# Performance work log

Measured on AMD Instinct MI355X. Metric: run time of the kernel, lower is better.

The kernel has to match this reference:

```python
import jax, jax.numpy as jnp
import numpy as np

B = 65536
D_EMB = 512      # embedding_dim
D_SPD = 1        # speed_dim
D_LAT = 128      # speed_latent_dim
H = 256          # hidden_size
K = 6            # num_branch
D_IN = D_EMB + D_LAT  # 640, branch/speed-head input dim


def _lin(key, din, dout):
    kw, kb = jax.random.split(key)
    W = jax.random.normal(kw, (din, dout), dtype=jnp.float32) * 0.02
    b = jax.random.normal(kb, (dout,), dtype=jnp.float32) * 0.02
    return W, b


def setup_inputs() -> dict:
    key = jax.random.key(0)
    ks = jax.random.split(key, 16)
    embedding = jax.random.normal(ks[0], (B, D_EMB), dtype=jnp.float32)
    speed = jax.random.uniform(ks[1], (B, D_SPD), dtype=jnp.float32)
    command = jax.random.randint(ks[2], (B,), 1, K + 1, dtype=jnp.int32)  # values 1..6
    # speed input MLP: speed_dim -> H -> D_LAT
    Wsi1, bsi1 = _lin(ks[3], D_SPD, H)
    Wsi2, bsi2 = _lin(ks[4], H, D_LAT)
    # speed prediction head: D_IN -> H -> H -> speed_dim
    Wso1, bso1 = _lin(ks[5], D_IN, H)
    Wso2, bso2 = _lin(ks[6], H, H)
    Wso3, bso3 = _lin(ks[7], H, D_SPD)
    # K branch heads, stacked on leading axis: D_IN -> H -> H -> 3, sigmoid
    def _stack(key, din, dout):
        kw, kb = jax.random.split(key)
        W = jax.random.normal(kw, (K, din, dout), dtype=jnp.float32) * 0.02
        b = jax.random.normal(kb, (K, dout), dtype=jnp.float32) * 0.02
        return W, b
    Wb1, bb1 = _stack(ks[8], D_IN, H)
    Wb2, bb2 = _stack(ks[9], H, H)
    Wb3, bb3 = _stack(ks[10], H, 3)
    return dict(embedding=embedding, speed=speed, command=command,
                Wsi1=Wsi1, bsi1=bsi1, Wsi2=Wsi2, bsi2=bsi2,
                Wso1=Wso1, bso1=bso1, Wso2=Wso2, bso2=bso2, Wso3=Wso3, bso3=bso3,
                Wb1=Wb1, bb1=bb1, Wb2=Wb2, bb2=bb2, Wb3=Wb3, bb3=bb3)


def reference(embedding, speed, command,
              Wsi1, bsi1, Wsi2, bsi2,
              Wso1, bso1, Wso2, bso2, Wso3, bso3,
              Wb1, bb1, Wb2, bb2, Wb3, bb3):
    # speed -> latent
    sp = jax.nn.relu(speed @ Wsi1 + bsi1) @ Wsi2 + bsi2          # [B, D_LAT]
    emb = jnp.concatenate([embedding, sp], axis=1)               # [B, D_IN]
    # compute ALL K branch heads (as the original does), then mask by command
    h = jax.nn.relu(jnp.einsum('bd,kdh->bkh', emb, Wb1) + bb1)   # [B, K, H]
    h = jax.nn.relu(jnp.einsum('bkh,khj->bkj', h, Wb2) + bb2)    # [B, K, H]
    ctrl_all = jax.nn.sigmoid(jnp.einsum('bkh,kho->bko', h, Wb3) + bb3)  # [B, K, 3]
    mask = (command[:, None] - 1 == jnp.arange(K)[None, :]).astype(ctrl_all.dtype)  # [B, K]
    control_pred = jnp.sum(ctrl_all * mask[:, :, None], axis=1)  # [B, 3]
    # speed prediction head
    hs = jax.nn.relu(emb @ Wso1 + bso1)
    hs = jax.nn.relu(hs @ Wso2 + bso2)
    speed_pred = hs @ Wso3 + bso3                                # [B, 1]
    return control_pred, speed_pred
```

## Files before the change

kernel.cpp:

```cpp
#include <hip/hip_runtime.h>
#include <hip/hip_bf16.h>


#define NB 65536
#define NBRB 1030

typedef __attribute__((ext_vector_type(8))) short short8;
typedef __attribute__((ext_vector_type(4))) float f32x4;
typedef unsigned short bhalf;
typedef unsigned int u32;

__device__ __forceinline__ bhalf f2b(float x) {
    __hip_bfloat16 h = __float2bfloat16(x);
    return *reinterpret_cast<bhalf*>(&h);
}
__device__ __forceinline__ void gll16(const void* g, void* l) {
    __builtin_amdgcn_global_load_lds(
        (const __attribute__((address_space(1))) u32*)g,
        (__attribute__((address_space(3))) u32*)l, 16, 0, 0);
}
__device__ __forceinline__ int sadr(int row, int cb) {
    return row * 64 + (cb ^ (((row >> 1) & 3) << 4));
}
__device__ __forceinline__ int yadr(int row, int cb) {
    return row * 512 + (cb ^ ((row & 7) << 4));
}
__device__ __forceinline__ void wvm6() { asm volatile("s_waitcnt vmcnt(6)" ::: "memory"); }
__device__ __forceinline__ void wvm0() { asm volatile("s_waitcnt vmcnt(0)" ::: "memory"); }
__device__ __forceinline__ void wlgkm0() { asm volatile("s_waitcnt lgkmcnt(0)" ::: "memory"); }

__global__ __launch_bounds__(256) void k_wprep(
    const float* __restrict__ Wsi2, const float* __restrict__ Wso1,
    const float* __restrict__ Wso2, const float* __restrict__ Wb1,
    const float* __restrict__ Wb2,
    bhalf* __restrict__ Wsi2T, bhalf* __restrict__ Wso1T,
    bhalf* __restrict__ Wso2T, bhalf* __restrict__ Wb1T,
    bhalf* __restrict__ Wb2T) {
    __shared__ float T[64][65];
    const int id = blockIdx.x, t = threadIdx.x;
    const float* src; bhalf* dst; int K, N, tk, tn, b;
    if (id < 8)        { src = Wsi2; dst = Wsi2T; K = 256; N = 128; b = 0; int tl = id;      tk = tl / 2; tn = tl % 2; }
    else if (id < 48)  { src = Wso1; dst = Wso1T; K = 640; N = 256; b = 0; int tl = id - 8;  tk = tl / 4; tn = tl % 4; }
    else if (id < 64)  { src = Wso2; dst = Wso2T; K = 256; N = 256; b = 0; int tl = id - 48; tk = tl / 4; tn = tl % 4; }
    else if (id < 304) { src = Wb1;  dst = Wb1T;  K = 640; N = 256; int li = id - 64;  b = li / 40; int tl = li % 40; tk = tl / 4; tn = tl % 4; }
    else               { src = Wb2;  dst = Wb2T;  K = 256; N = 256; int li = id - 304; b = li / 16; int tl = li % 16; tk = tl / 4; tn = tl % 4; }
    const int k0 = tk * 64, n0 = tn * 64;
    src += (size_t)b * K * N; dst += (size_t)b * N * K;
    const int c = t & 63, r0 = t >> 6;
#pragma unroll
    for (int j = 0; j < 16; ++j) {
        int r = r0 + j * 4;
        T[r][c] = src[(size_t)(k0 + r) * N + n0 + c];
    }
    __syncthreads();
#pragma unroll
    for (int j = 0; j < 16; ++j) {
        int r = r0 + j * 4;
        dst[(size_t)(n0 + r) * K + k0 + c] = f2b(T[c][r]);
    }
}

__global__ __launch_bounds__(256) void k_prep(
    const float* __restrict__ speed, const float* __restrict__ Wsi1,
    const float* __restrict__ bsi1, const bhalf* __restrict__ Wsi2T,
    const float* __restrict__ bsi2, const int* __restrict__ cmd,
    bhalf* __restrict__ spb, int* __restrict__ bcnt) {
    __shared__ bhalf A[64 * 72];
    __shared__ bhalf BT[128 * 72];
    const int t = threadIdx.x, lane = t & 63, wid = t >> 6;
    const int rbase = blockIdx.x * 64;
    if (wid == 0) {
        int c = cmd[rbase + lane] - 1;
        int v = 0;
#pragma unroll
        for (int g = 0; g < 6; ++g) {
            unsigned long long m = __ballot(c == g);
            if (lane == g) v = (int)__popcll(m);
        }
        if (lane < 6) bcnt[blockIdx.x * 6 + lane] = v;
    }
    const int wm = wid >> 1, wn = wid & 1;
    f32x4 acc[2][4];
    for (int m = 0; m < 2; ++m) for (int n = 0; n < 4; ++n)
        for (int r = 0; r < 4; ++r) acc[m][n][r] = 0.f;
    const int ar = t >> 2, kp = (t & 3) * 16;
    const float s = speed[rbase + ar];
    for (int kc = 0; kc < 4; ++kc) {
        short8 w0, w1;
#pragma unroll
        for (int j = 0; j < 8; ++j) {
            int k = kc * 64 + kp + j;
            w0[j] = (short)f2b(fmaxf(fmaf(s, Wsi1[k], bsi1[k]), 0.f));
            w1[j] = (short)f2b(fmaxf(fmaf(s, Wsi1[k + 8], bsi1[k + 8]), 0.f));
        }
        *(short8*)&A[ar * 72 + kp] = w0;
        *(short8*)&A[ar * 72 + kp + 8] = w1;
#pragma unroll
        for (int j = 0; j < 4; ++j) {
            int ch = t + j * 256;
            int n2 = ch >> 3, ko = (ch & 7) * 8;
            *(short8*)&BT[n2 * 72 + ko] =
                *(const short8*)(Wsi2T + n2 * 256 + kc * 64 + ko);
        }
        __syncthreads();
#pragma unroll
        for (int ks = 0; ks < 2; ++ks) {
            short8 a[2], b[4];
#pragma unroll
            for (int m = 0; m < 2; ++m)
                a[m] = *(const short8*)&A[(wm * 32 + m * 16 + (lane & 15)) * 72 + ks * 32 + (lane >> 4) * 8];
#pragma unroll
            for (int n = 0; n < 4; ++n)
                b[n] = *(const short8*)&BT[(wn * 64 + n * 16 + (lane & 15)) * 72 + ks * 32 + (lane >> 4) * 8];
#pragma unroll
            for (int m = 0; m < 2; ++m)
#pragma unroll
                for (int n = 0; n < 4; ++n)
                    acc[m][n] = __builtin_amdgcn_mfma_f32_16x16x32_bf16(a[m], b[n], acc[m][n], 0, 0, 0);
        }
        __syncthreads();
    }
#pragma unroll
    for (int m = 0; m < 2; ++m)
#pragma unroll
    for (int n = 0; n < 4; ++n) {
        int col = wn * 64 + n * 16 + (lane & 15);
        float bias = bsi2[col];
#pragma unroll
        for (int r = 0; r < 4; ++r) {
            int row = rbase + wm * 32 + m * 16 + (lane >> 4) * 4 + r;
            spb[row * 128 + col] = f2b(acc[m][n][r] + bias);
        }
    }
}

__global__ __launch_bounds__(1024) void k_scan(
    const int* __restrict__ bcnt, int* __restrict__ chunkoff,
    int* __restrict__ pad) {
    __shared__ int sc[1024];
    __shared__ int tot[8];
    __shared__ int spo[8];
    const int t = threadIdx.x;
    for (int g = 0; g < 6; ++g) {
        int v = bcnt[t * 6 + g];
        sc[t] = v;
        __syncthreads();
        for (int s = 1; s < 1024; s <<= 1) {
            int u = (t >= s) ? sc[t - s] : 0;
            __syncthreads();
            sc[t] += u;
            __syncthreads();
        }
        if (t == 1023) tot[g] = sc[t];
        chunkoff[t * 6 + g] = sc[t] - v;
        __syncthreads();
    }
    if (t == 0) {
        int off = 0;
        for (int g = 0; g < 6; ++g) {
            spo[g] = off; pad[g] = off; pad[8 + g] = tot[g];
            off += ((tot[g] + 63) >> 6) << 6;
        }
        spo[6] = off; pad[6] = off;
    }
    __syncthreads();
    for (int g = 0; g < 6; ++g) chunkoff[t * 6 + g] += spo[g];
}

__global__ __launch_bounds__(256) void k_scatter(
    const int* __restrict__ cmd, const int* __restrict__ chunkoff,
    int* __restrict__ perm) {
    const int lane = threadIdx.x & 63, w = threadIdx.x >> 6;
    const int chunk = blockIdx.x * 4 + w;
    const int idx = chunk * 64 + lane;
    const int c = cmd[idx] - 1;
#pragma unroll
    for (int g = 0; g < 6; ++g) {
        unsigned long long m = __ballot(c == g);
        if (c == g) {
            int pos = chunkoff[chunk * 6 + g] + (int)__popcll(m & ((1ull << lane) - 1ull));
            perm[pos] = idx;
        }
    }
}

__global__ __launch_bounds__(256, 3) void k_head(
    const float* __restrict__ emb, const bhalf* __restrict__ spb,
    const bhalf* __restrict__ Wso1T, const float* __restrict__ bso1,
    const bhalf* __restrict__ Wso2T, const float* __restrict__ bso2,
    const float* __restrict__ Wso3, const float* __restrict__ bso3,
    const bhalf* __restrict__ Wb1T, const float* __restrict__ bb1,
    const bhalf* __restrict__ Wb2T, const float* __restrict__ bb2,
    const float* __restrict__ Wb3, const float* __restrict__ bb3,
    const int* __restrict__ pad, const int* __restrict__ perm,
    float* __restrict__ out) {
    __shared__ __align__(16) char L[49152];
    char* const SB0 = L;
    char* const SAr = L + 32768;
    char* const Yb  = L;
    const int t = threadIdx.x, lane = t & 63, wid = t >> 6;
    const bool isB = blockIdx.x < NBRB;
    int tstart, DOUT, gcnt, gbase;
    const bhalf *W1T, *W2T; const float *b1, *b2, *W3, *b3;
    if (isB) {
        tstart = blockIdx.x * 64;
        if (tstart >= pad[6]) return;
        int g = 0;
        while (pad[g + 1] <= tstart) ++g;
        gbase = pad[g]; gcnt = pad[8 + g];
        W1T = Wb1T + (size_t)g * (256 * 640); b1 = bb1 + g * 256;
        W2T = Wb2T + (size_t)g * (256 * 256); b2 = bb2 + g * 256;
        W3  = Wb3  + (size_t)g * (256 * 3);   b3 = bb3 + g * 3;
        DOUT = 3;
    } else {
        tstart = (blockIdx.x - NBRB) * 64;
        gbase = 0; gcnt = NB;
        W1T = Wso1T; b1 = bso1; W2T = Wso2T; b2 = bso2; W3 = Wso3; b3 = bso3;
        DOUT = 1;
    }

    const int rowA0 = t >> 3, rowA1 = rowA0 + 32, rowS = t >> 2;
    int ra0, ra1, raS;
    if (isB) {
        int p0 = tstart + rowA0, p1 = tstart + rowA1, pS = tstart + rowS;
        ra0 = ((p0 - gbase) < gcnt) ? perm[p0] : 0;
        ra1 = ((p1 - gbase) < gcnt) ? perm[p1] : 0;
        raS = ((pS - gbase) < gcnt) ? perm[pS] : 0;
    } else {
        ra0 = tstart + rowA0; ra1 = tstart + rowA1; raS = tstart + rowS;
    }
    const int lcA0 = ((t & 7) * 16) ^ ((rowA0 & 7) << 4);
    const int lcA1 = ((t & 7) * 16) ^ ((rowA1 & 7) << 4);
    const int lcS  = ((t & 3) * 16) ^ (((rowS >> 1) & 3) << 4);
    const char* embp0 = (const char*)(emb + (size_t)ra0 * 512);
    const char* embp1 = (const char*)(emb + (size_t)ra1 * 512);
    const char* spbp  = (const char*)(spb + (size_t)raS * 128);
    const int dstA = t * 16;
    const int rB = t >> 2, cB = (t & 3) * 16;

#define ST_A(KN, BUF) do { int kn_ = (KN); char* d_ = SAr + (BUF) * 8192 + dstA; \
        if (kn_ < 16) {                                                           \
            gll16(embp0 + kn_ * 128 + lcA0, d_);                                  \
            gll16(embp1 + kn_ * 128 + lcA1, d_ + 4096);                           \
        } else {                                                                  \
            gll16(spbp + (kn_ - 16) * 64 + lcS, d_);                              \
            gll16(spbp + (kn_ - 16) * 64 + lcS, d_ + 4096);                       \
        } } while (0)
#define ST_B1(KN, BUF) do {                                                       \
        _Pragma("unroll")                                                         \
        for (int j_ = 0; j_ < 4; ++j_) {                                          \
            int row_ = rB + j_ * 64;                                              \
            int p_ = row_ * 64 + cB;                                              \
            int lc_ = cB ^ (((row_ >> 1) & 3) << 4);                              \
            gll16((const char*)W1T + (size_t)row_ * 1280 + (KN) * 64 + lc_,       \
                  SB0 + (BUF) * 16384 + p_);                                      \
        } } while (0)
#define ST_B2(KB) do {                                                            \
        _Pragma("unroll")                                                         \
        for (int j_ = 0; j_ < 4; ++j_) {                                          \
            int row_ = rB + j_ * 64;                                              \
            int p_ = row_ * 64 + cB;                                              \
            int lc_ = cB ^ (((row_ >> 1) & 3) << 4);                              \
            gll16((const char*)W2T + (size_t)row_ * 512 + (KB) + lc_,             \
                  SAr + p_);                                                      \
        } } while (0)

    const int arow = lane & 15, koff = (lane >> 4) * 16;
    float bi1[4], bi2[4];
#pragma unroll
    for (int n = 0; n < 4; ++n) {
        bi1[n] = b1[wid * 64 + n * 16 + arow];
        bi2[n] = b2[wid * 64 + n * 16 + arow];
    }

    f32x4 acc[4][4];
#pragma unroll
    for (int m = 0; m < 4; ++m)
#pragma unroll
        for (int n = 0; n < 4; ++n)
#pragma unroll
            for (int r = 0; r < 4; ++r) acc[m][n][r] = 0.f;

    ST_A(0, 0); ST_B1(0, 0);
    for (int kc = 0; kc < 20; ++kc) {
        const int buf = kc & 1;
        if (kc < 19) { ST_A(kc + 1, buf ^ 1); ST_B1(kc + 1, buf ^ 1); wvm6(); }
        else         { wvm0(); }
        __builtin_amdgcn_s_barrier();
        const char* SAc = SAr + buf * 8192;
        const char* SBc = SB0 + buf * 16384;
        short8 a[4], b[4];
#pragma unroll
        for (int n = 0; n < 4; ++n)
            b[n] = *(const short8*)(SBc + sadr(wid * 64 + n * 16 + arow, koff));
        if (kc < 16) {
#pragma unroll
            for (int m = 0; m < 4; ++m) {
                int row = m * 16 + arow;
                int sw = (row & 7) << 4;
                int c0 = (lane >> 4) * 32;
                float4 f0 = *(const float4*)(SAc + row * 128 + (c0 ^ sw));
                float4 f1 = *(const float4*)(SAc + row * 128 + ((c0 + 16) ^ sw));
                a[m][0] = (short)f2b(f0.x); a[m][1] = (short)f2b(f0.y);
                a[m][2] = (short)f2b(f0.z); a[m][3] = (short)f2b(f0.w);
                a[m][4] = (short)f2b(f1.x); a[m][5] = (short)f2b(f1.y);
                a[m][6] = (short)f2b(f1.z); a[m][7] = (short)f2b(f1.w);
            }
        } else {
#pragma unroll
            for (int m = 0; m < 4; ++m)
                a[m] = *(const short8*)(SAc + sadr(m * 16 + arow, koff));
        }
#pragma unroll
        for (int m = 0; m < 4; ++m)
#pragma unroll
            for (int n = 0; n < 4; ++n)
                acc[m][n] = __builtin_amdgcn_mfma_f32_16x16x32_bf16(a[m], b[n], acc[m][n], 0, 0, 0);
        __builtin_amdgcn_s_barrier();
    }
#pragma unroll
    for (int m = 0; m < 4; ++m)
#pragma unroll
    for (int n = 0; n < 4; ++n) {
        int col = wid * 64 + n * 16 + arow;
#pragma unroll
        for (int r = 0; r < 4; ++r) {
            int row = m * 16 + (lane >> 4) * 4 + r;
            *(bhalf*)(Yb + yadr(row, 2 * col)) = f2b(fmaxf(acc[m][n][r] + bi1[n], 0.f));
            acc[m][n][r] = 0.f;
        }
    }
    ST_B2(0);
    wlgkm0();
    wvm0();
    __builtin_amdgcn_s_barrier();
    for (int kc = 0; kc < 8; ++kc) {
        short8 a[4], b[4];
#pragma unroll
        for (int m = 0; m < 4; ++m)
            a[m] = *(const short8*)(Yb + yadr(m * 16 + arow, kc * 64 + koff));
#pragma unroll
        for (int n = 0; n < 4; ++n)
            b[n] = *(const short8*)(SAr + sadr(wid * 64 + n * 16 + arow, koff));
#pragma unroll
        for (int m = 0; m < 4; ++m)
#pragma unroll
            for (int n = 0; n < 4; ++n)
                acc[m][n] = __builtin_amdgcn_mfma_f32_16x16x32_bf16(a[m], b[n], acc[m][n], 0, 0, 0);
        __builtin_amdgcn_s_barrier();
        if (kc < 7) { ST_B2((kc + 1) * 64); wvm0(); }
        __builtin_amdgcn_s_barrier();
    }
#pragma unroll
    for (int m = 0; m < 4; ++m)
#pragma unroll
    for (int n = 0; n < 4; ++n) {
        int col = wid * 64 + n * 16 + arow;
#pragma unroll
        for (int r = 0; r < 4; ++r) {
            int row = m * 16 + (lane >> 4) * 4 + r;
            *(bhalf*)(Yb + yadr(row, 2 * col)) = f2b(fmaxf(acc[m][n][r] + bi2[n], 0.f));
        }
    }
    wlgkm0();
    __builtin_amdgcn_s_barrier();
    f32x4 z;
#pragma unroll
    for (int r = 0; r < 4; ++r) z[r] = 0.f;
    const int col3 = arow;
    for (int kc = 0; kc < 8; ++kc) {
        short8 a3 = *(const short8*)(Yb + yadr(wid * 16 + arow, kc * 64 + koff));
        short8 bw;
#pragma unroll
        for (int j = 0; j < 8; ++j) bw[j] = 0;
        if (col3 < DOUT) {
            int kb = kc * 32 + (lane >> 4) * 8;
#pragma unroll
            for (int j = 0; j < 8; ++j)
                bw[j] = (short)f2b(W3[(kb + j) * DOUT + col3]);
        }
        z = __builtin_amdgcn_mfma_f32_16x16x32_bf16(a3, bw, z, 0, 0, 0);
    }
    if (col3 < DOUT) {
        float bias = b3[col3];
#pragma unroll
        for (int rr = 0; rr < 4; ++rr) {
            int r = wid * 16 + (lane >> 4) * 4 + rr;
            int p2 = tstart + r;
            if ((p2 - gbase) < gcnt) {
                float v = z[rr] + bias;
                if (isB) {
                    int ro = perm[p2];
                    out[(size_t)ro * 3 + col3] = 1.f / (1.f + __expf(-v));
                } else {
                    out[(size_t)NB * 3 + p2] = v;
                }
            }
        }
    }
#undef ST_A
#undef ST_B1
#undef ST_B2
}

extern "C" void kernel_launch(void* const* d_in, const int* in_sizes, int n_in,
                              void* d_out, int out_size, void* d_ws, size_t ws_size,
                              hipStream_t stream) {
    (void)in_sizes; (void)n_in; (void)out_size; (void)ws_size;
    const float* emb   = (const float*)d_in[0];
    const float* speed = (const float*)d_in[1];
    const int*   cmd   = (const int*)d_in[2];
    const float* Wsi1  = (const float*)d_in[3];
    const float* bsi1  = (const float*)d_in[4];
    const float* Wsi2  = (const float*)d_in[5];
    const float* bsi2  = (const float*)d_in[6];
    const float* Wso1  = (const float*)d_in[7];
    const float* bso1  = (const float*)d_in[8];
    const float* Wso2  = (const float*)d_in[9];
    const float* bso2  = (const float*)d_in[10];
    const float* Wso3  = (const float*)d_in[11];
    const float* bso3  = (const float*)d_in[12];
    const float* Wb1   = (const float*)d_in[13];
    const float* bb1   = (const float*)d_in[14];
    const float* Wb2   = (const float*)d_in[15];
    const float* bb2   = (const float*)d_in[16];
    const float* Wb3   = (const float*)d_in[17];
    const float* bb3   = (const float*)d_in[18];
    float* out = (float*)d_out;

    char* ws = (char*)d_ws;
    bhalf* spb      = (bhalf*)(ws);
    int*   perm     = (int*)(ws + 16777216);
    int*   bcnt     = (int*)(ws + 17040896);
    int*   chunkoff = (int*)(ws + 17065472);
    int*   pad      = (int*)(ws + 17090048);
    bhalf* Wsi2T    = (bhalf*)(ws + 17090304);
    bhalf* Wso1T    = (bhalf*)(ws + 17155840);
    bhalf* Wso2T    = (bhalf*)(ws + 17483520);
    bhalf* Wb1T     = (bhalf*)(ws + 17614592);
    bhalf* Wb2T     = (bhalf*)(ws + 19580672);

    k_wprep<<<400, 256, 0, stream>>>(Wsi2, Wso1, Wso2, Wb1, Wb2,
                                     Wsi2T, Wso1T, Wso2T, Wb1T, Wb2T);
    k_prep<<<NB / 64, 256, 0, stream>>>(speed, Wsi1, bsi1, Wsi2T, bsi2, cmd,
                                        spb, bcnt);
    k_scan<<<1, 1024, 0, stream>>>(bcnt, chunkoff, pad);
    k_scatter<<<NB / 256, 256, 0, stream>>>(cmd, chunkoff, perm);
    k_head<<<NBRB + NB / 64, 256, 0, stream>>>(emb, spb,
                                               Wso1T, bso1, Wso2T, bso2, Wso3, bso3,
                                               Wb1T, bb1, Wb2T, bb2, Wb3, bb3,
                                               pad, perm, out);
}
```

Measured before the change: 155.7 us.

## Share embedding tile loads between branch and speed heads, split into two persistent kernels

The single head kernel ran separate blocks for the branch MLP and the speed MLP, so each embedding row was loaded and converted twice. Now one block computes both first-layer GEMMs (branch and speed weights side by side, N=512) over the permuted row order. It writes the bf16 hidden activations to a global scratch buffer, and a second persistent kernel runs layers 2 and 3 for both heads. This removes the duplicate reads of the fp32 embedding. The cost is a 128 MB round-trip of intermediates, more LDS, occupancy dropping from 3 to 2 blocks, and a launch split into two grid-strided persistent grids.

```diff
diff --git a/kernel.cpp b/kernel.cpp
--- a/kernel.cpp
+++ b/kernel.cpp
@@ -3,7 +3,7 @@
 
 
 #define NB 65536
-#define NBRB 1030
+#define KGRID 1024
 
 typedef __attribute__((ext_vector_type(8))) short short8;
 typedef __attribute__((ext_vector_type(4))) float f32x4;
@@ -22,12 +22,12 @@
 __device__ __forceinline__ int sadr(int row, int cb) {
     return row * 64 + (cb ^ (((row >> 1) & 3) << 4));
 }
-__device__ __forceinline__ int yadr(int row, int cb) {
-    return row * 512 + (cb ^ ((row & 7) << 4));
-}
-__device__ __forceinline__ void wvm6() { asm volatile("s_waitcnt vmcnt(6)" ::: "memory"); }
-__device__ __forceinline__ void wvm0() { asm volatile("s_waitcnt vmcnt(0)" ::: "memory"); }
-__device__ __forceinline__ void wlgkm0() { asm volatile("s_waitcnt lgkmcnt(0)" ::: "memory"); }
+__device__ __forceinline__ int yadr2(int row, int cb) {
+    return row * 1024 + (cb ^ ((row & 7) << 4));
+}
+__device__ __forceinline__ void wvm10() { asm volatile("s_waitcnt vmcnt(10)" ::: "memory"); }
+__device__ __forceinline__ void wvm0()  { asm volatile("s_waitcnt vmcnt(0)"  ::: "memory"); }
+__device__ __forceinline__ void wlgkm0(){ asm volatile("s_waitcnt lgkmcnt(0)" ::: "memory"); }
 
 __global__ __launch_bounds__(256) void k_wprep(
     const float* __restrict__ Wsi2, const float* __restrict__ Wso1,
@@ -184,61 +184,41 @@
     }
 }
 
-__global__ __launch_bounds__(256, 3) void k_head(
+__global__ __launch_bounds__(256, 2) void k1(
     const float* __restrict__ emb, const bhalf* __restrict__ spb,
     const bhalf* __restrict__ Wso1T, const float* __restrict__ bso1,
-    const bhalf* __restrict__ Wso2T, const float* __restrict__ bso2,
-    const float* __restrict__ Wso3, const float* __restrict__ bso3,
     const bhalf* __restrict__ Wb1T, const float* __restrict__ bb1,
-    const bhalf* __restrict__ Wb2T, const float* __restrict__ bb2,
-    const float* __restrict__ Wb3, const float* __restrict__ bb3,
     const int* __restrict__ pad, const int* __restrict__ perm,
-    float* __restrict__ out) {
-    __shared__ __align__(16) char L[49152];
-    char* const SB0 = L;
-    char* const SAr = L + 32768;
-    char* const Yb  = L;
+    bhalf* __restrict__ Yg) {
+    __shared__ __align__(16) char L[81920];
+    char* const SA0 = L;
+    char* const SB0 = L + 16384;
     const int t = threadIdx.x, lane = t & 63, wid = t >> 6;
-    const bool isB = blockIdx.x < NBRB;
-    int tstart, DOUT, gcnt, gbase;
-    const bhalf *W1T, *W2T; const float *b1, *b2, *W3, *b3;
-    if (isB) {
-        tstart = blockIdx.x * 64;
-        if (tstart >= pad[6]) return;
-        int g = 0;
-        while (pad[g + 1] <= tstart) ++g;
-        gbase = pad[g]; gcnt = pad[8 + g];
-        W1T = Wb1T + (size_t)g * (256 * 640); b1 = bb1 + g * 256;
-        W2T = Wb2T + (size_t)g * (256 * 256); b2 = bb2 + g * 256;
-        W3  = Wb3  + (size_t)g * (256 * 3);   b3 = bb3 + g * 3;
-        DOUT = 3;
-    } else {
-        tstart = (blockIdx.x - NBRB) * 64;
-        gbase = 0; gcnt = NB;
-        W1T = Wso1T; b1 = bso1; W2T = Wso2T; b2 = bso2; W3 = Wso3; b3 = bso3;
-        DOUT = 1;
-    }
-
+    const int pad6 = pad[6];
+    const int arow = lane & 15, koff = (lane >> 4) * 16;
     const int rowA0 = t >> 3, rowA1 = rowA0 + 32, rowS = t >> 2;
-    int ra0, ra1, raS;
-    if (isB) {
-        int p0 = tstart + rowA0, p1 = tstart + rowA1, pS = tstart + rowS;
-        ra0 = ((p0 - gbase) < gcnt) ? perm[p0] : 0;
-        ra1 = ((p1 - gbase) < gcnt) ? perm[p1] : 0;
-        raS = ((pS - gbase) < gcnt) ? perm[pS] : 0;
-    } else {
-        ra0 = tstart + rowA0; ra1 = tstart + rowA1; raS = tstart + rowS;
-    }
     const int lcA0 = ((t & 7) * 16) ^ ((rowA0 & 7) << 4);
     const int lcA1 = ((t & 7) * 16) ^ ((rowA1 & 7) << 4);
     const int lcS  = ((t & 3) * 16) ^ (((rowS >> 1) & 3) << 4);
-    const char* embp0 = (const char*)(emb + (size_t)ra0 * 512);
-    const char* embp1 = (const char*)(emb + (size_t)ra1 * 512);
-    const char* spbp  = (const char*)(spb + (size_t)raS * 128);
     const int dstA = t * 16;
     const int rB = t >> 2, cB = (t & 3) * 16;
 
-#define ST_A(KN, BUF) do { int kn_ = (KN); char* d_ = SAr + (BUF) * 8192 + dstA; \
+    for (int tile = blockIdx.x; tile * 64 < pad6; tile += KGRID) {
+        const int tstart = tile * 64;
+        int g = 0;
+        while (pad[g + 1] <= tstart) ++g;
+        const int gbase = pad[g], gcnt = pad[8 + g];
+        const bhalf* W1b = Wb1T + (size_t)g * (256 * 640);
+
+        int p0 = tstart + rowA0, p1 = tstart + rowA1, pS = tstart + rowS;
+        const int ra0 = ((p0 - gbase) < gcnt) ? perm[p0] : 0;
+        const int ra1 = ((p1 - gbase) < gcnt) ? perm[p1] : 0;
+        const int raS = ((pS - gbase) < gcnt) ? perm[pS] : 0;
+        const char* embp0 = (const char*)(emb + (size_t)ra0 * 512);
+        const char* embp1 = (const char*)(emb + (size_t)ra1 * 512);
+        const char* spbp  = (const char*)(spb + (size_t)raS * 128);
+
+#define ST_A(KN, BUF) do { int kn_ = (KN); char* d_ = SA0 + (BUF) * 8192 + dstA; \
         if (kn_ < 16) {                                                           \
             gll16(embp0 + kn_ * 128 + lcA0, d_);                                  \
             gll16(embp1 + kn_ * 128 + lcA1, d_ + 4096);                           \
@@ -246,161 +226,245 @@
             gll16(spbp + (kn_ - 16) * 64 + lcS, d_);                              \
             gll16(spbp + (kn_ - 16) * 64 + lcS, d_ + 4096);                       \
         } } while (0)
-#define ST_B1(KN, BUF) do {                                                       \
+#define ST_B(KN, BUF) do {                                                        \
         _Pragma("unroll")                                                         \
         for (int j_ = 0; j_ < 4; ++j_) {                                          \
             int row_ = rB + j_ * 64;                                              \
             int p_ = row_ * 64 + cB;                                              \
             int lc_ = cB ^ (((row_ >> 1) & 3) << 4);                              \
-            gll16((const char*)W1T + (size_t)row_ * 1280 + (KN) * 64 + lc_,       \
-                  SB0 + (BUF) * 16384 + p_);                                      \
+            gll16((const char*)W1b + (size_t)row_ * 1280 + (KN) * 64 + lc_,       \
+                  SB0 + (BUF) * 32768 + p_);                                      \
+            gll16((const char*)Wso1T + (size_t)row_ * 1280 + (KN) * 64 + lc_,     \
+                  SB0 + (BUF) * 32768 + 16384 + p_);                              \
         } } while (0)
-#define ST_B2(KB) do {                                                            \
+
+        float bi1[8];
+#pragma unroll
+        for (int n = 0; n < 4; ++n) {
+            bi1[n]     = bb1[g * 256 + wid * 64 + n * 16 + arow];
+            bi1[n + 4] = bso1[wid * 64 + n * 16 + arow];
+        }
+
+        f32x4 acc[4][8];
+#pragma unroll
+        for (int m = 0; m < 4; ++m)
+#pragma unroll
+            for (int n = 0; n < 8; ++n)
+#pragma unroll
+                for (int r = 0; r < 4; ++r) acc[m][n][r] = 0.f;
+
+        ST_A(0, 0); ST_B(0, 0);
+        for (int kc = 0; kc < 20; ++kc) {
+            const int buf = kc & 1;
+            if (kc < 19) { ST_A(kc + 1, buf ^ 1); ST_B(kc + 1, buf ^ 1); wvm10(); }
+            else         { wvm0(); }
+            __builtin_amdgcn_s_barrier();
+            const char* SAc = SA0 + buf * 8192;
+            const char* SBc = SB0 + buf * 32768;
+            short8 a[4], b[8];
+#pragma unroll
+            for (int n = 0; n < 4; ++n) {
+                b[n]     = *(const short8*)(SBc + sadr(wid * 64 + n * 16 + arow, koff));
+                b[n + 4] = *(const short8*)(SBc + 16384 + sadr(wid * 64 + n * 16 + arow, koff));
+            }
+            if (kc < 16) {
+#pragma unroll
+                for (int m = 0; m < 4; ++m) {
+                    int row = m * 16 + arow;
+                    int sw = (row & 7) << 4;
+                    int c0 = (lane >> 4) * 32;
+                    float4 f0 = *(const float4*)(SAc + row * 128 + (c0 ^ sw));
+                    float4 f1 = *(const float4*)(SAc + row * 128 + ((c0 + 16) ^ sw));
+                    a[m][0] = (short)f2b(f0.x); a[m][1] = (short)f2b(f0.y);
+                    a[m][2] = (short)f2b(f0.z); a[m][3] = (short)f2b(f0.w);
+                    a[m][4] = (short)f2b(f1.x); a[m][5] = (short)f2b(f1.y);
+                    a[m][6] = (short)f2b(f1.z); a[m][7] = (short)f2b(f1.w);
+                }
+            } else {
+#pragma unroll
+                for (int m = 0; m < 4; ++m)
+                    a[m] = *(const short8*)(SAc + sadr(m * 16 + arow, koff));
+            }
+#pragma unroll
+            for (int m = 0; m < 4; ++m)
+#pragma unroll
+                for (int n = 0; n < 8; ++n)
+                    acc[m][n] = __builtin_amdgcn_mfma_f32_16x16x32_bf16(a[m], b[n], acc[m][n], 0, 0, 0);
+            __builtin_amdgcn_s_barrier();
+        }
+#pragma unroll
+        for (int m = 0; m < 4; ++m)
+#pragma unroll
+        for (int n = 0; n < 8; ++n) {
+            int col = (n < 4) ? (wid * 64 + n * 16 + arow)
+                              : (256 + wid * 64 + (n - 4) * 16 + arow);
+#pragma unroll
+            for (int r = 0; r < 4; ++r) {
+                int row = m * 16 + (lane >> 4) * 4 + r;
+                *(bhalf*)(L + yadr2(row, 2 * col)) = f2b(fmaxf(acc[m][n][r] + bi1[n], 0.f));
+            }
+        }
+        wlgkm0();
+        __builtin_amdgcn_s_barrier();
+        char* Ygb = (char*)Yg + (size_t)tstart * 1024;
+#pragma unroll
+        for (int j = 0; j < 16; ++j) {
+            int p = t * 16 + j * 4096;
+            int row = p >> 10, cb = p & 1023;
+            uint4 v = *(const uint4*)(L + row * 1024 + (cb ^ ((row & 7) << 4)));
+            *(uint4*)(Ygb + (size_t)row * 1024 + cb) = v;
+        }
+        __syncthreads();
+#undef ST_A
+#undef ST_B
+    }
+}
+
+__global__ __launch_bounds__(256, 2) void k2(
+    const bhalf* __restrict__ Yg,
+    const bhalf* __restrict__ Wso2T, const float* __restrict__ bso2,
+    const float* __restrict__ Wso3, const float* __restrict__ bso3,
+    const bhalf* __restrict__ Wb2T, const float* __restrict__ bb2,
+    const float* __restrict__ Wb3, const float* __restrict__ bb3,
+    const int* __restrict__ pad, const int* __restrict__ perm,
+    float* __restrict__ out) {
+    __shared__ __align__(16) char L[81920];
+    char* const SA0 = L;
+    char* const SB0 = L + 16384;
+    const int t = threadIdx.x, lane = t & 63, wid = t >> 6;
+    const int pad6 = pad[6];
+    const int arow = lane & 15, koff = (lane >> 4) * 16;
+    const int rowY = t >> 2, cA = (t & 3) * 16;
+    const int lcA = cA ^ (((rowY >> 1) & 3) << 4);
+    const int dstA = t * 16;
+    const int rB = t >> 2, cB = (t & 3) * 16;
+
+    for (int tile = blockIdx.x; tile * 64 < pad6; tile += KGRID) {
+        const int tstart = tile * 64;
+        int g = 0;
+        while (pad[g + 1] <= tstart) ++g;
+        const int gbase = pad[g], gcnt = pad[8 + g];
+        const bhalf* W2b = Wb2T + (size_t)g * (256 * 256);
+        const float* W3b = Wb3 + (size_t)g * (256 * 3);
+        const float* b3b = bb3 + g * 3;
+        const char* ygp = (const char*)Yg + (size_t)(tstart + rowY) * 1024;
+
+#define ST_A2(KC, BUF) do { char* d_ = SA0 + (BUF) * 8192 + dstA;                \
+        gll16(ygp + (KC) * 64 + lcA, d_);                                         \
+        gll16(ygp + 512 + (KC) * 64 + lcA, d_ + 4096);                            \
+    } while (0)
+#define ST_B2(KC, BUF) do {                                                       \
         _Pragma("unroll")                                                         \
         for (int j_ = 0; j_ < 4; ++j_) {                                          \
             int row_ = rB + j_ * 64;                                              \
             int p_ = row_ * 64 + cB;                                              \
             int lc_ = cB ^ (((row_ >> 1) & 3) << 4);                              \
-            gll16((const char*)W2T + (size_t)row_ * 512 + (KB) + lc_,             \
-                  SAr + p_);                                                      \
+            gll16((const char*)W2b + (size_t)row_ * 512 + (KC) * 64 + lc_,        \
+                  SB0 + (BUF) * 32768 + p_);                                      \
+            gll16((const char*)Wso2T + (size_t)row_ * 512 + (KC) * 64 + lc_,      \
+                  SB0 + (BUF) * 32768 + 16384 + p_);                              \
         } } while (0)
 
-    const int arow = lane & 15, koff = (lane >> 4) * 16;
-    float bi1[4], bi2[4];
-#pragma unroll
-    for (int n = 0; n < 4; ++n) {
-        bi1[n] = b1[wid * 64 + n * 16 + arow];
-        bi2[n] = b2[wid * 64 + n * 16 + arow];
-    }
-
-    f32x4 acc[4][4];
-#pragma unroll
-    for (int m = 0; m < 4; ++m)
-#pragma unroll
-        for (int n = 0; n < 4; ++n)
-#pragma unroll
-            for (int r = 0; r < 4; ++r) acc[m][n][r] = 0.f;
-
-    ST_A(0, 0); ST_B1(0, 0);
-    for (int kc = 0; kc < 20; ++kc) {
-        const int buf = kc & 1;
-        if (kc < 19) { ST_A(kc + 1, buf ^ 1); ST_B1(kc + 1, buf ^ 1); wvm6(); }
-        else         { wvm0(); }
+        float bi2[8];
+#pragma unroll
+        for (int n = 0; n < 4; ++n) {
+            bi2[n]     = bb2[g * 256 + wid * 64 + n * 16 + arow];
+            bi2[n + 4] = bso2[wid * 64 + n * 16 + arow];
+        }
+
+        f32x4 acc[4][8];
+#pragma unroll
+        for (int m = 0; m < 4; ++m)
+#pragma unroll
+            for (int n = 0; n < 8; ++n)
+#pragma unroll
+                for (int r = 0; r < 4; ++r) acc[m][n][r] = 0.f;
+
+        ST_A2(0, 0); ST_B2(0, 0);
+        for (int kc = 0; kc < 8; ++kc) {
+            const int buf = kc & 1;
+            if (kc < 7) { ST_A2(kc + 1, buf ^ 1); ST_B2(kc + 1, buf ^ 1); wvm10(); }
+            else        { wvm0(); }
+            __builtin_amdgcn_s_barrier();
+            const char* SAc = SA0 + buf * 8192;
+            const char* SBc = SB0 + buf * 32768;
+            short8 aB[4], aS[4], b[8];
+#pragma unroll
+            for (int m = 0; m < 4; ++m) {
+                aB[m] = *(const short8*)(SAc + sadr(m * 16 + arow, koff));
+                aS[m] = *(const short8*)(SAc + 4096 + sadr(m * 16 + arow, koff));
+            }
+#pragma unroll
+            for (int n = 0; n < 4; ++n) {
+                b[n]     = *(const short8*)(SBc + sadr(wid * 64 + n * 16 + arow, koff));
+                b[n + 4] = *(const short8*)(SBc + 16384 + sadr(wid * 64 + n * 16 + arow, koff));
+            }
+#pragma unroll
+            for (int m = 0; m < 4; ++m)
+#pragma unroll
+                for (int n = 0; n < 4; ++n) {
+                    acc[m][n]     = __builtin_amdgcn_mfma_f32_16x16x32_bf16(aB[m], b[n],     acc[m][n],     0, 0, 0);
+                    acc[m][n + 4] = __builtin_amdgcn_mfma_f32_16x16x32_bf16(aS[m], b[n + 4], acc[m][n + 4], 0, 0, 0);
+                }
+            __builtin_amdgcn_s_barrier();
+        }
+#pragma unroll
+        for (int m = 0; m < 4; ++m)
+#pragma unroll
+        for (int n = 0; n < 8; ++n) {
+            int col = (n < 4) ? (wid * 64 + n * 16 + arow)
+                              : (256 + wid * 64 + (n - 4) * 16 + arow);
+#pragma unroll
+            for (int r = 0; r < 4; ++r) {
+                int row = m * 16 + (lane >> 4) * 4 + r;
+                *(bhalf*)(L + yadr2(row, 2 * col)) = f2b(fmaxf(acc[m][n][r] + bi2[n], 0.f));
+            }
+        }
+        wlgkm0();
         __builtin_amdgcn_s_barrier();
-        const char* SAc = SAr + buf * 8192;
-        const char* SBc = SB0 + buf * 16384;
-        short8 a[4], b[4];
-#pragma unroll
-        for (int n = 0; n < 4; ++n)
-            b[n] = *(const short8*)(SBc + sadr(wid * 64 + n * 16 + arow, koff));
-        if (kc < 16) {
-#pragma unroll
-            for (int m = 0; m < 4; ++m) {
-                int row = m * 16 + arow;
-                int sw = (row & 7) << 4;
-                int c0 = (lane >> 4) * 32;
-                float4 f0 = *(const float4*)(SAc + row * 128 + (c0 ^ sw));
-                float4 f1 = *(const float4*)(SAc + row * 128 + ((c0 + 16) ^ sw));
-                a[m][0] = (short)f2b(f0.x); a[m][1] = (short)f2b(f0.y);
-                a[m][2] = (short)f2b(f0.z); a[m][3] = (short)f2b(f0.w);
-                a[m][4] = (short)f2b(f1.x); a[m][5] = (short)f2b(f1.y);
-                a[m][6] = (short)f2b(f1.z); a[m][7] = (short)f2b(f1.w);
-            }
-        } else {
-#pragma unroll
-            for (int m = 0; m < 4; ++m)
-                a[m] = *(const short8*)(SAc + sadr(m * 16 + arow, koff));
-        }
-#pragma unroll
-        for (int m = 0; m < 4; ++m)
-#pragma unroll
-            for (int n = 0; n < 4; ++n)
-                acc[m][n] = __builtin_amdgcn_mfma_f32_16x16x32_bf16(a[m], b[n], acc[m][n], 0, 0, 0);
-        __builtin_amdgcn_s_barrier();
-    }
-#pragma unroll
-    for (int m = 0; m < 4; ++m)
-#pragma unroll
-    for (int n = 0; n < 4; ++n) {
-        int col = wid * 64 + n * 16 + arow;
-#pragma unroll
-        for (int r = 0; r < 4; ++r) {
-            int row = m * 16 + (lane >> 4) * 4 + r;
-            *(bhalf*)(Yb + yadr(row, 2 * col)) = f2b(fmaxf(acc[m][n][r] + bi1[n], 0.f));
-            acc[m][n][r] = 0.f;
-        }
-    }
-    ST_B2(0);
-    wlgkm0();
-    wvm0();
-    __builtin_amdgcn_s_barrier();
-    for (int kc = 0; kc < 8; ++kc) {
-        short8 a[4], b[4];
-#pragma unroll
-        for (int m = 0; m < 4; ++m)
-            a[m] = *(const short8*)(Yb + yadr(m * 16 + arow, kc * 64 + koff));
-#pragma unroll
-        for (int n = 0; n < 4; ++n)
-            b[n] = *(const short8*)(SAr + sadr(wid * 64 + n * 16 + arow, koff));
-#pragma unroll
-        for (int m = 0; m < 4; ++m)
-#pragma unroll
-            for (int n = 0; n < 4; ++n)
-                acc[m][n] = __builtin_amdgcn_mfma_f32_16x16x32_bf16(a[m], b[n], acc[m][n], 0, 0, 0);
-        __builtin_amdgcn_s_barrier();
-        if (kc < 7) { ST_B2((kc + 1) * 64); wvm0(); }
-        __builtin_amdgcn_s_barrier();
-    }
-#pragma unroll
-    for (int m = 0; m < 4; ++m)
-#pragma unroll
-    for (int n = 0; n < 4; ++n) {
-        int col = wid * 64 + n * 16 + arow;
-#pragma unroll
-        for (int r = 0; r < 4; ++r) {
-            int row = m * 16 + (lane >> 4) * 4 + r;
-            *(bhalf*)(Yb + yadr(row, 2 * col)) = f2b(fmaxf(acc[m][n][r] + bi2[n], 0.f));
-        }
-    }
-    wlgkm0();
-    __builtin_amdgcn_s_barrier();
-    f32x4 z;
-#pragma unroll
-    for (int r = 0; r < 4; ++r) z[r] = 0.f;
-    const int col3 = arow;
-    for (int kc = 0; kc < 8; ++kc) {
-        short8 a3 = *(const short8*)(Yb + yadr(wid * 16 + arow, kc * 64 + koff));
-        short8 bw;
-#pragma unroll
-        for (int j = 0; j < 8; ++j) bw[j] = 0;
-        if (col3 < DOUT) {
+        f32x4 zB, zS;
+#pragma unroll
+        for (int r = 0; r < 4; ++r) { zB[r] = 0.f; zS[r] = 0.f; }
+        const int col3 = arow;
+        for (int kc = 0; kc < 8; ++kc) {
+            short8 a3b = *(const short8*)(L + yadr2(wid * 16 + arow, kc * 64 + koff));
+            short8 a3s = *(const short8*)(L + yadr2(wid * 16 + arow, 512 + kc * 64 + koff));
+            short8 bwB, bwS;
+#pragma unroll
+            for (int j = 0; j < 8; ++j) { bwB[j] = 0; bwS[j] = 0; }
             int kb = kc * 32 + (lane >> 4) * 8;
-#pragma unroll
-            for (int j = 0; j < 8; ++j)
-                bw[j] = (short)f2b(W3[(kb + j) * DOUT + col3]);
-        }
-        z = __builtin_amdgcn_mfma_f32_16x16x32_bf16(a3, bw, z, 0, 0, 0);
-    }
-    if (col3 < DOUT) {
-        float bias = b3[col3];
+            if (col3 < 3) {
+#pragma unroll
+                for (int j = 0; j < 8; ++j)
+                    bwB[j] = (short)f2b(W3b[(kb + j) * 3 + col3]);
+            }
+            if (col3 < 1) {
+#pragma unroll
+                for (int j = 0; j < 8; ++j)
+                    bwS[j] = (short)f2b(Wso3[kb + j]);
+            }
+            zB = __builtin_amdgcn_mfma_f32_16x16x32_bf16(a3b, bwB, zB, 0, 0, 0);
+            zS = __builtin_amdgcn_mfma_f32_16x16x32_bf16(a3s, bwS, zS, 0, 0, 0);
+        }
 #pragma unroll
         for (int rr = 0; rr < 4; ++rr) {
             int r = wid * 16 + (lane >> 4) * 4 + rr;
             int p2 = tstart + r;
             if ((p2 - gbase) < gcnt) {
-                float v = z[rr] + bias;
-                if (isB) {
-                    int ro = perm[p2];
+                int ro = perm[p2];
+                if (col3 < 3) {
+                    float v = zB[rr] + b3b[col3];
                     out[(size_t)ro * 3 + col3] = 1.f / (1.f + __expf(-v));
-                } else {
-                    out[(size_t)NB * 3 + p2] = v;
                 }
-            }
-        }
-    }
-#undef ST_A
-#undef ST_B1
+                if (col3 < 1) {
+                    out[(size_t)NB * 3 + ro] = zS[rr] + bso3[0];
+                }
+            }
+        }
+        __syncthreads();
+#undef ST_A2
 #undef ST_B2
+    }
 }
 
 extern "C" void kernel_launch(void* const* d_in, const int* in_sizes, int n_in,
@@ -439,6 +503,7 @@
     bhalf* Wso2T    = (bhalf*)(ws + 17483520);
     bhalf* Wb1T     = (bhalf*)(ws + 17614592);
     bhalf* Wb2T     = (bhalf*)(ws + 19580672);
+    bhalf* Yg       = (bhalf*)(ws + 20367104);
 
     k_wprep<<<400, 256, 0, stream>>>(Wsi2, Wso1, Wso2, Wb1, Wb2,
                                      Wsi2T, Wso1T, Wso2T, Wb1T, Wb2T);
@@ -446,8 +511,8 @@
                                         spb, bcnt);
     k_scan<<<1, 1024, 0, stream>>>(bcnt, chunkoff, pad);
     k_scatter<<<NB / 256, 256, 0, stream>>>(cmd, chunkoff, perm);
-    k_head<<<NBRB + NB / 64, 256, 0, stream>>>(emb, spb,
-                                               Wso1T, bso1, Wso2T, bso2, Wso3, bso3,
-                                               Wb1T, bb1, Wb2T, bb2, Wb3, bb3,
-                                               pad, perm, out);
-}
+    k1<<<KGRID, 256, 0, stream>>>(emb, spb, Wso1T, bso1, Wb1T, bb1,
+                                  pad, perm, Yg);
+    k2<<<KGRID, 256, 0, stream>>>(Yg, Wso2T, bso2, Wso3, bso3,
+                                  Wb2T, bb2, Wb3, bb3, pad, perm, out);
+}
```

Result: slower. 340.3 us (+118.6%).
